# Performance work log

Hardware: AMD Instinct MI355X
Metric: run time of the kernel (lower is better)

The kernel has to match this reference:

```python
import jax, jax.numpy as jnp
import numpy as np

DIM = 64  # per-head dim used for the sqrt scale


def setup_inputs() -> dict:
    key = jax.random.key(0)
    kq, kk, kv, ke, kf = jax.random.split(key, 5)
    B, N, d, k = 32, 4096, 64, 256
    Q = jax.random.normal(kq, (B, N, d), dtype=jnp.float32)
    K = jax.random.normal(kk, (B, N, d), dtype=jnp.float32)
    V = jax.random.normal(kv, (B, N, d), dtype=jnp.float32)
    E = jax.random.normal(ke, (N, k), dtype=jnp.float32) * (1.0 / np.sqrt(N))
    F = jax.random.normal(kf, (N, k), dtype=jnp.float32) * (1.0 / np.sqrt(N))
    return {"Q": Q, "K": K, "V": V, "E": E, "F": F}


def reference(Q, K, V, E, F):
    # Linformer head: K^T E -> [B,d,k]; Q (K^T E) / sqrt(d) -> [B,N,k]
    K_proj = jnp.einsum('bnd,nk->bdk', K, E)          # low-rank key projection
    scores = jnp.einsum('bnd,bdk->bnk', Q, K_proj) / jnp.sqrt(jnp.float32(DIM))
    P_bar = jax.nn.softmax(scores, axis=2)            # [B,N,k]
    # (V^T F)^T -> [B,k,d]
    V_proj = jnp.einsum('bnd,nk->bkd', V, F)
    return jnp.einsum('bnk,bkd->bnd', P_bar, V_proj)  # [B,N,d]
```

## Files before the change

kernel.cpp:

```cpp
#include <hip/hip_runtime.h>
#include <hip/hip_bf16.h>

#define BB 32
#define NN 4096
#define DDIM 64
#define KKR 256

typedef __attribute__((ext_vector_type(8)))  short bf16x8;
typedef __attribute__((ext_vector_type(16))) float f32x16;
typedef __attribute__((ext_vector_type(4)))  float f32x4;

static __device__ inline unsigned short f2bf(float x) {
  union { float f; unsigned u; } v; v.f = x;
  unsigned r = (v.u + 0x7FFFu + ((v.u >> 16) & 1u)) >> 16;
  return (unsigned short)r;
}

__global__ __launch_bounds__(256) void pass0_kernel(
    const float* __restrict__ K, const float* __restrict__ V,
    const float* __restrict__ E, const float* __restrict__ F,
    unsigned short* __restrict__ KT, unsigned short* __restrict__ VT,
    unsigned short* __restrict__ ET, unsigned short* __restrict__ FT)
{
  const int id = blockIdx.x;
  const int t  = threadIdx.x;
  const float* src; unsigned short* dst; int stride, n0, col0;
  if (id < 2048) {
    int b = id >> 6, nt = id & 63;
    src = K + (long)b * NN * DDIM; dst = KT + (long)b * DDIM * NN;
    stride = 64; n0 = nt * 64; col0 = 0;
  } else if (id < 4096) {
    int i2 = id - 2048; int b = i2 >> 6, nt = i2 & 63;
    src = V + (long)b * NN * DDIM; dst = VT + (long)b * DDIM * NN;
    stride = 64; n0 = nt * 64; col0 = 0;
  } else if (id < 4352) {
    int i2 = id - 4096; int nt = i2 >> 2, ct = i2 & 3;
    src = E; dst = ET; stride = 256; n0 = nt * 64; col0 = ct * 64;
  } else {
    int i2 = id - 4352; int nt = i2 >> 2, ct = i2 & 3;
    src = F; dst = FT; stride = 256; n0 = nt * 64; col0 = ct * 64;
  }
  const int c = t & 63;
  const int q = t >> 6;
  const float* sp = src + (long)(n0 + q * 16) * stride + col0 + c;
  float v[16];
#pragma unroll
  for (int j = 0; j < 16; ++j) v[j] = sp[(long)j * stride];
  unsigned short o[16];
#pragma unroll
  for (int j = 0; j < 16; ++j) o[j] = f2bf(v[j]);
  unsigned short* dp = dst + (long)(col0 + c) * NN + n0 + q * 16;
#pragma unroll
  for (int j4 = 0; j4 < 4; ++j4)
    *(ushort4*)(dp + j4 * 4) = *(const ushort4*)&o[j4 * 4];
}

__global__ __launch_bounds__(256, 2) void proj_gemm(
    const unsigned short* __restrict__ KT, const unsigned short* __restrict__ VT,
    const unsigned short* __restrict__ ET, const unsigned short* __restrict__ FT,
    float* __restrict__ KpP, float* __restrict__ VpP)
{
  extern __shared__ unsigned short sm[];
  const int blk = blockIdx.x;
  const int chunk = blk & 3, mat = (blk >> 2) & 1, b = blk >> 3;
  const int t = threadIdx.x, w = t >> 6, l = t & 63, h = l >> 5, lr = l & 31;

  const unsigned short *Ag, *Bg; int M; float* Cg;
  if (mat == 0) {
    Ag = ET; Bg = KT + (long)b * DDIM * NN; M = 256;
    Cg = KpP + (long)chunk * (BB * 16384) + b * 16384;
  } else {
    Ag = VT + (long)b * DDIM * NN; Bg = FT; M = 64;
    Cg = VpP + (long)chunk * (BB * 16384) + b * 16384;
  }
  const int mt0 = (mat == 0) ? 2 * w : 0;
  const int nt0 = (mat == 0) ? 0 : 2 * w;

  f32x16 acc[2][2];
#pragma unroll
  for (int i = 0; i < 2; ++i)
#pragma unroll
    for (int j = 0; j < 2; ++j)
#pragma unroll
      for (int q = 0; q < 16; ++q) acc[i][j][q] = 0.f;

  const int n0 = chunk * 1024;
  for (int stg = 0; stg < 16; ++stg) {
    const int nb = n0 + stg * 64;
    __syncthreads();
#pragma unroll
    for (int i = 0; i < 10; ++i) {
      int cidx = i * 256 + t;
      int row = cidx >> 3, off = cidx & 7;
      const unsigned short* g =
          (row < M ? Ag + (long)row * NN : Bg + (long)(row - M) * NN) + nb + off * 8;
      *(bf16x8*)&sm[row * 72 + off * 8] = *(const bf16x8*)g;
    }
    __syncthreads();
#pragma unroll
    for (int kk = 0; kk < 4; ++kk) {
      bf16x8 a0 = *(const bf16x8*)&sm[(mt0 * 32 + lr) * 72 + kk * 16 + h * 8];
      bf16x8 a1 = *(const bf16x8*)&sm[((mt0 + 1) * 32 + lr) * 72 + kk * 16 + h * 8];
      bf16x8 b0 = *(const bf16x8*)&sm[(M + nt0 * 32 + lr) * 72 + kk * 16 + h * 8];
      bf16x8 b1 = *(const bf16x8*)&sm[(M + (nt0 + 1) * 32 + lr) * 72 + kk * 16 + h * 8];
      acc[0][0] = __builtin_amdgcn_mfma_f32_32x32x16_bf16(a0, b0, acc[0][0], 0, 0, 0);
      acc[0][1] = __builtin_amdgcn_mfma_f32_32x32x16_bf16(a0, b1, acc[0][1], 0, 0, 0);
      acc[1][0] = __builtin_amdgcn_mfma_f32_32x32x16_bf16(a1, b0, acc[1][0], 0, 0, 0);
      acc[1][1] = __builtin_amdgcn_mfma_f32_32x32x16_bf16(a1, b1, acc[1][1], 0, 0, 0);
    }
  }
#pragma unroll
  for (int mt = 0; mt < 2; ++mt)
#pragma unroll
    for (int nt = 0; nt < 2; ++nt)
#pragma unroll
      for (int i = 0; i < 16; ++i) {
        int row = (mt0 + mt) * 32 + (i & 3) + 8 * (i >> 2) + 4 * h;
        int col = (nt0 + nt) * 32 + lr;
        int idx = (mat == 0) ? row * 64 + col : row * 256 + col;
        Cg[idx] = acc[mt][nt][i];
      }
}

__global__ __launch_bounds__(256) void reduce_cvt(
    const float* __restrict__ KpP, const float* __restrict__ VpP,
    unsigned short* __restrict__ Kpb, unsigned short* __restrict__ Vpb)
{
  const int blk = blockIdx.x;
  const float* src = (blk < 256) ? KpP : VpP;
  unsigned short* dst = (blk < 256) ? Kpb : Vpb;
  const long i = (long)(blk & 255) * 2048 + threadIdx.x * 8;
  float a[8];
#pragma unroll
  for (int j = 0; j < 8; ++j) a[j] = 0.f;
#pragma unroll
  for (int cch = 0; cch < 4; ++cch) {
    const float4 p0 = *(const float4*)(src + (long)cch * (BB * 16384) + i);
    const float4 p1 = *(const float4*)(src + (long)cch * (BB * 16384) + i + 4);
    a[0] += p0.x; a[1] += p0.y; a[2] += p0.z; a[3] += p0.w;
    a[4] += p1.x; a[5] += p1.y; a[6] += p1.z; a[7] += p1.w;
  }
  unsigned short o[8];
#pragma unroll
  for (int j = 0; j < 8; ++j) o[j] = f2bf(a[j]);
  *(bf16x8*)(dst + i) = *(const bf16x8*)&o[0];
}

__global__ __launch_bounds__(256, 2) void attn2_kernel(
    const float* __restrict__ Qg, const unsigned short* __restrict__ Kpb,
    const unsigned short* __restrict__ Vpb, float* __restrict__ Og)
{
  extern __shared__ char smraw[];
  unsigned short* P = (unsigned short*)smraw;
  float* scr = (float*)(smraw + 65536);
  float* red = (float*)(smraw + 65536 + 8192);

  const int blk = blockIdx.x;
  const int b = blk >> 5, rg = blk & 31;
  const int t = threadIdx.x, w = t >> 6, l = t & 63, h = l >> 5, lr = l & 31;
  const int rh = w >> 1, ch = w & 1;

  const float* Qbase = Qg + ((long)b * NN + rg * 128) * 64;
  bf16x8 A[2][4];
#pragma unroll
  for (int rt = 0; rt < 2; ++rt)
#pragma unroll
    for (int kk = 0; kk < 4; ++kk) {
      const float* qp = Qbase + (long)(rh * 64 + rt * 32 + lr) * 64 + kk * 16 + h * 8;
      float4 x = *(const float4*)qp;
      float4 y = *(const float4*)(qp + 4);
      unsigned short u[8];
      u[0] = f2bf(x.x); u[1] = f2bf(x.y); u[2] = f2bf(x.z); u[3] = f2bf(x.w);
      u[4] = f2bf(y.x); u[5] = f2bf(y.y); u[6] = f2bf(y.z); u[7] = f2bf(y.w);
      A[rt][kk] = *(const bf16x8*)u;
    }

  const unsigned short* Kp = Kpb + (long)b * 16384;
  f32x16 acc[2][4];
#pragma unroll
  for (int rt = 0; rt < 2; ++rt)
#pragma unroll
    for (int ct = 0; ct < 4; ++ct)
#pragma unroll
      for (int q = 0; q < 16; ++q) acc[rt][ct][q] = 0.f;

  bf16x8 Bf[4], Bn[4];
#pragma unroll
  for (int ct = 0; ct < 4; ++ct)
    Bf[ct] = *(const bf16x8*)(Kp + (long)(ch * 128 + ct * 32 + lr) * 64 + h * 8);
#pragma unroll
  for (int kk = 0; kk < 4; ++kk) {
    if (kk < 3) {
#pragma unroll
      for (int ct = 0; ct < 4; ++ct)
        Bn[ct] = *(const bf16x8*)(Kp + (long)(ch * 128 + ct * 32 + lr) * 64 + (kk + 1) * 16 + h * 8);
    }
#pragma unroll
    for (int ct = 0; ct < 4; ++ct) {
      acc[0][ct] = __builtin_amdgcn_mfma_f32_32x32x16_bf16(A[0][kk], Bf[ct], acc[0][ct], 0, 0, 0);
      acc[1][ct] = __builtin_amdgcn_mfma_f32_32x32x16_bf16(A[1][kk], Bf[ct], acc[1][ct], 0, 0, 0);
    }
#pragma unroll
    for (int ct = 0; ct < 4; ++ct) Bf[ct] = Bn[ct];
  }

#pragma unroll
  for (int rt = 0; rt < 2; ++rt)
#pragma unroll
    for (int ct = 0; ct < 4; ++ct)
#pragma unroll
      for (int q = 0; q < 16; ++q)
        acc[rt][ct][q] = exp2f(acc[rt][ct][q] * 0.1803368801f);

  float ps[2][16];
#pragma unroll
  for (int rt = 0; rt < 2; ++rt)
#pragma unroll
    for (int q = 0; q < 16; ++q)
      ps[rt][q] = (acc[rt][0][q] + acc[rt][1][q]) + (acc[rt][2][q] + acc[rt][3][q]);
#pragma unroll
  for (int rt = 0; rt < 2; ++rt)
#pragma unroll
    for (int q = 0; q < 16; ++q) {
      ps[rt][q] += __shfl_xor(ps[rt][q], 8);
      ps[rt][q] += __shfl_xor(ps[rt][q], 16);
    }
  if (((l >> 3) & 3) == 0) {
#pragma unroll
    for (int rt = 0; rt < 2; ++rt)
#pragma unroll
      for (int q = 0; q < 16; ++q) {
        int rowL = (q & 3) + 8 * (q >> 2) + 4 * h;
        scr[w * 512 + (rt * 32 + rowL) * 8 + (l & 7)] = ps[rt][q];
      }
  }
  {
    const float* p = &scr[w * 512 + l * 8];
    f32x4 x = *(const f32x4*)p, y = *(const f32x4*)(p + 4);
    float s = (x[0] + x[1]) + (x[2] + x[3]) + (y[0] + y[1]) + (y[2] + y[3]);
    red[ch * 128 + rh * 64 + l] = s;
  }

#pragma unroll
  for (int rt = 0; rt < 2; ++rt)
#pragma unroll
    for (int ct = 0; ct < 4; ++ct)
#pragma unroll
      for (int q = 0; q < 16; ++q) {
        int rowL = rh * 64 + rt * 32 + (q & 3) + 8 * (q >> 2) + 4 * h;
        int col  = ch * 128 + ct * 32 + lr;
        int chk  = (col >> 3) ^ (rowL & 7);
        P[rowL * 256 + chk * 8 + (col & 7)] = f2bf(acc[rt][ct][q]);
      }
  __syncthreads();

  const unsigned short* Vp = Vpb + (long)b * 16384;
  f32x16 o[2];
#pragma unroll
  for (int rt = 0; rt < 2; ++rt)
#pragma unroll
    for (int q = 0; q < 16; ++q) o[rt][q] = 0.f;

#pragma unroll
  for (int kk = 0; kk < 16; ++kk) {
    bf16x8 Bv = *(const bf16x8*)(Vp + (long)(ch * 32 + lr) * 256 + kk * 16 + h * 8);
    bf16x8 Ap[2];
#pragma unroll
    for (int rt = 0; rt < 2; ++rt) {
      int rowL = rh * 64 + rt * 32 + lr;
      int col  = kk * 16 + h * 8;
      int chk  = (col >> 3) ^ (rowL & 7);
      Ap[rt] = *(const bf16x8*)&P[rowL * 256 + chk * 8];
    }
    o[0] = __builtin_amdgcn_mfma_f32_32x32x16_bf16(Ap[0], Bv, o[0], 0, 0, 0);
    o[1] = __builtin_amdgcn_mfma_f32_32x32x16_bf16(Ap[1], Bv, o[1], 0, 0, 0);
  }

#pragma unroll
  for (int rt = 0; rt < 2; ++rt)
#pragma unroll
    for (int ig = 0; ig < 4; ++ig) {
      int r0 = rh * 64 + rt * 32 + ig * 8 + 4 * h;
      f32x4 l0 = *(const f32x4*)&red[r0];
      f32x4 l1 = *(const f32x4*)&red[128 + r0];
#pragma unroll
      for (int j = 0; j < 4; ++j) {
        float val = o[rt][ig * 4 + j] * __builtin_amdgcn_rcpf(l0[j] + l1[j]);
        Og[((long)b * NN + rg * 128 + r0 + j) * 64 + ch * 32 + lr] = val;
      }
    }
}

extern "C" void kernel_launch(void* const* d_in, const int* in_sizes, int n_in,
                              void* d_out, int out_size, void* d_ws, size_t ws_size,
                              hipStream_t stream) {
  const float* Q = (const float*)d_in[0];
  const float* K = (const float*)d_in[1];
  const float* V = (const float*)d_in[2];
  const float* E = (const float*)d_in[3];
  const float* F = (const float*)d_in[4];
  float* out = (float*)d_out;

  char* ws = (char*)d_ws;
  float*          KpP = (float*)(ws);
  float*          VpP = (float*)(ws + (8l << 20));
  unsigned short* Kpb = (unsigned short*)(ws + (16l << 20));
  unsigned short* Vpb = (unsigned short*)(ws + (17l << 20));
  unsigned short* KT  = (unsigned short*)(ws + (18l << 20));
  unsigned short* VT  = (unsigned short*)(ws + (34l << 20));
  unsigned short* ET  = (unsigned short*)(ws + (50l << 20));
  unsigned short* FT  = (unsigned short*)(ws + (52l << 20));

  pass0_kernel<<<dim3(4608), dim3(256), 0, stream>>>(K, V, E, F, KT, VT, ET, FT);

  hipFuncSetAttribute((const void*)proj_gemm,
                      hipFuncAttributeMaxDynamicSharedMemorySize, 46080);
  proj_gemm<<<dim3(256), dim3(256), 46080, stream>>>(KT, VT, ET, FT, KpP, VpP);

  reduce_cvt<<<dim3(512), dim3(256), 0, stream>>>(KpP, VpP, Kpb, Vpb);

  hipFuncSetAttribute((const void*)attn2_kernel,
                      hipFuncAttributeMaxDynamicSharedMemorySize, 74752);
  attn2_kernel<<<dim3(1024), dim3(256), 74752, stream>>>(Q, Kpb, Vpb, out);
}
```

Before: 214.2 us.

## Keep attention probabilities in registers via transposed MFMA and coalesce output

Restructures the attention kernel so each wave owns 32 full rows, computing S^T = Kp·Q^T so that the exp'd probabilities can be repacked into bf16 MFMA operands with cross-half shuffles instead of a large LDS staging buffer. The row sum becomes a per-lane accumulation plus one shuffle, which removes the scratch reductions and the mid-kernel barrier. Output is staged through a swizzled LDS tile so global stores are float4-coalesced. The pass0 transpose store also uses 16-byte writes. The cost is a higher register footprint from holding 16 bf16x8 P fragments, and each wave now reloads all of Kp and Vp from global or cache.

```diff
diff --git a/kernel.cpp b/kernel.cpp
--- a/kernel.cpp
+++ b/kernel.cpp
@@ -14,6 +14,13 @@
   union { float f; unsigned u; } v; v.f = x;
   unsigned r = (v.u + 0x7FFFu + ((v.u >> 16) & 1u)) >> 16;
   return (unsigned short)r;
+}
+
+static __device__ inline unsigned packbf2(float a, float b) {
+  union { float f; unsigned u; } x, y; x.f = a; y.f = b;
+  unsigned ua = x.u + 0x7FFFu + ((x.u >> 16) & 1u);
+  unsigned ub = y.u + 0x7FFFu + ((y.u >> 16) & 1u);
+  return (ua >> 16) | (ub & 0xFFFF0000u);
 }
 
 __global__ __launch_bounds__(256) void pass0_kernel(
@@ -50,9 +57,8 @@
 #pragma unroll
   for (int j = 0; j < 16; ++j) o[j] = f2bf(v[j]);
   unsigned short* dp = dst + (long)(col0 + c) * NN + n0 + q * 16;
-#pragma unroll
-  for (int j4 = 0; j4 < 4; ++j4)
-    *(ushort4*)(dp + j4 * 4) = *(const ushort4*)&o[j4 * 4];
+  *(bf16x8*)dp       = *(const bf16x8*)&o[0];
+  *(bf16x8*)(dp + 8) = *(const bf16x8*)&o[8];
 }
 
 __global__ __launch_bounds__(256, 2) void proj_gemm(
@@ -150,145 +156,106 @@
     const float* __restrict__ Qg, const unsigned short* __restrict__ Kpb,
     const unsigned short* __restrict__ Vpb, float* __restrict__ Og)
 {
-  extern __shared__ char smraw[];
-  unsigned short* P = (unsigned short*)smraw;
-  float* scr = (float*)(smraw + 65536);
-  float* red = (float*)(smraw + 65536 + 8192);
+  __shared__ float O_lds[128 * 64];
 
   const int blk = blockIdx.x;
   const int b = blk >> 5, rg = blk & 31;
-  const int t = threadIdx.x, w = t >> 6, l = t & 63, h = l >> 5, lr = l & 31;
-  const int rh = w >> 1, ch = w & 1;
-
-  const float* Qbase = Qg + ((long)b * NN + rg * 128) * 64;
-  bf16x8 A[2][4];
-#pragma unroll
-  for (int rt = 0; rt < 2; ++rt)
+  const int t = threadIdx.x, w = t >> 6, l = t & 63;
+  const int h = l >> 5, lr = l & 31;
+  const int rbase = rg * 128 + w * 32;
+
+  const float* Qrow = Qg + ((long)b * NN + rbase + lr) * 64;
+  bf16x8 Bq[4];
+#pragma unroll
+  for (int kk = 0; kk < 4; ++kk) {
+    float4 x = *(const float4*)(Qrow + kk * 16 + h * 8);
+    float4 y = *(const float4*)(Qrow + kk * 16 + h * 8 + 4);
+    unsigned short u[8];
+    u[0] = f2bf(x.x); u[1] = f2bf(x.y); u[2] = f2bf(x.z); u[3] = f2bf(x.w);
+    u[4] = f2bf(y.x); u[5] = f2bf(y.y); u[6] = f2bf(y.z); u[7] = f2bf(y.w);
+    Bq[kk] = *(const bf16x8*)u;
+  }
+
+  const unsigned short* Kp = Kpb + (long)b * 16384;
+  const unsigned short* Vp = Vpb + (long)b * 16384;
+
+  union UV { uint4 u; bf16x8 v; };
+  bf16x8 Bp[16];
+  float rowpart = 0.f;
+
+#pragma unroll
+  for (int kt = 0; kt < 8; ++kt) {
+    f32x16 s;
+#pragma unroll
+    for (int q = 0; q < 16; ++q) s[q] = 0.f;
 #pragma unroll
     for (int kk = 0; kk < 4; ++kk) {
-      const float* qp = Qbase + (long)(rh * 64 + rt * 32 + lr) * 64 + kk * 16 + h * 8;
-      float4 x = *(const float4*)qp;
-      float4 y = *(const float4*)(qp + 4);
-      unsigned short u[8];
-      u[0] = f2bf(x.x); u[1] = f2bf(x.y); u[2] = f2bf(x.z); u[3] = f2bf(x.w);
-      u[4] = f2bf(y.x); u[5] = f2bf(y.y); u[6] = f2bf(y.z); u[7] = f2bf(y.w);
-      A[rt][kk] = *(const bf16x8*)u;
-    }
-
-  const unsigned short* Kp = Kpb + (long)b * 16384;
-  f32x16 acc[2][4];
-#pragma unroll
-  for (int rt = 0; rt < 2; ++rt)
-#pragma unroll
-    for (int ct = 0; ct < 4; ++ct)
-#pragma unroll
-      for (int q = 0; q < 16; ++q) acc[rt][ct][q] = 0.f;
-
-  bf16x8 Bf[4], Bn[4];
-#pragma unroll
-  for (int ct = 0; ct < 4; ++ct)
-    Bf[ct] = *(const bf16x8*)(Kp + (long)(ch * 128 + ct * 32 + lr) * 64 + h * 8);
-#pragma unroll
-  for (int kk = 0; kk < 4; ++kk) {
-    if (kk < 3) {
-#pragma unroll
-      for (int ct = 0; ct < 4; ++ct)
-        Bn[ct] = *(const bf16x8*)(Kp + (long)(ch * 128 + ct * 32 + lr) * 64 + (kk + 1) * 16 + h * 8);
-    }
-#pragma unroll
-    for (int ct = 0; ct < 4; ++ct) {
-      acc[0][ct] = __builtin_amdgcn_mfma_f32_32x32x16_bf16(A[0][kk], Bf[ct], acc[0][ct], 0, 0, 0);
-      acc[1][ct] = __builtin_amdgcn_mfma_f32_32x32x16_bf16(A[1][kk], Bf[ct], acc[1][ct], 0, 0, 0);
-    }
-#pragma unroll
-    for (int ct = 0; ct < 4; ++ct) Bf[ct] = Bn[ct];
-  }
-
-#pragma unroll
-  for (int rt = 0; rt < 2; ++rt)
-#pragma unroll
-    for (int ct = 0; ct < 4; ++ct)
-#pragma unroll
-      for (int q = 0; q < 16; ++q)
-        acc[rt][ct][q] = exp2f(acc[rt][ct][q] * 0.1803368801f);
-
-  float ps[2][16];
-#pragma unroll
-  for (int rt = 0; rt < 2; ++rt)
-#pragma unroll
-    for (int q = 0; q < 16; ++q)
-      ps[rt][q] = (acc[rt][0][q] + acc[rt][1][q]) + (acc[rt][2][q] + acc[rt][3][q]);
-#pragma unroll
-  for (int rt = 0; rt < 2; ++rt)
+      bf16x8 A = *(const bf16x8*)(Kp + (long)(kt * 32 + lr) * 64 + kk * 16 + h * 8);
+      s = __builtin_amdgcn_mfma_f32_32x32x16_bf16(A, Bq[kk], s, 0, 0, 0);
+    }
+    float p[16];
 #pragma unroll
     for (int q = 0; q < 16; ++q) {
-      ps[rt][q] += __shfl_xor(ps[rt][q], 8);
-      ps[rt][q] += __shfl_xor(ps[rt][q], 16);
-    }
-  if (((l >> 3) & 3) == 0) {
-#pragma unroll
-    for (int rt = 0; rt < 2; ++rt)
-#pragma unroll
-      for (int q = 0; q < 16; ++q) {
-        int rowL = (q & 3) + 8 * (q >> 2) + 4 * h;
-        scr[w * 512 + (rt * 32 + rowL) * 8 + (l & 7)] = ps[rt][q];
-      }
-  }
-  {
-    const float* p = &scr[w * 512 + l * 8];
-    f32x4 x = *(const f32x4*)p, y = *(const f32x4*)(p + 4);
-    float s = (x[0] + x[1]) + (x[2] + x[3]) + (y[0] + y[1]) + (y[2] + y[3]);
-    red[ch * 128 + rh * 64 + l] = s;
-  }
-
-#pragma unroll
-  for (int rt = 0; rt < 2; ++rt)
-#pragma unroll
-    for (int ct = 0; ct < 4; ++ct)
-#pragma unroll
-      for (int q = 0; q < 16; ++q) {
-        int rowL = rh * 64 + rt * 32 + (q & 3) + 8 * (q >> 2) + 4 * h;
-        int col  = ch * 128 + ct * 32 + lr;
-        int chk  = (col >> 3) ^ (rowL & 7);
-        P[rowL * 256 + chk * 8 + (col & 7)] = f2bf(acc[rt][ct][q]);
-      }
+      p[q] = exp2f(s[q] * 0.1803368801f);
+      rowpart += p[q];
+    }
+    unsigned wv[8];
+#pragma unroll
+    for (int m = 0; m < 8; ++m) wv[m] = packbf2(p[2 * m], p[2 * m + 1]);
+    unsigned r02 = __shfl_xor(h ? wv[0] : wv[2], 32);
+    unsigned r13 = __shfl_xor(h ? wv[1] : wv[3], 32);
+    unsigned r46 = __shfl_xor(h ? wv[4] : wv[6], 32);
+    unsigned r57 = __shfl_xor(h ? wv[5] : wv[7], 32);
+    UV c0, c1;
+    if (h == 0) {
+      c0.u = uint4{wv[0], wv[1], r02, r13};
+      c1.u = uint4{wv[4], wv[5], r46, r57};
+    } else {
+      c0.u = uint4{r02, r13, wv[2], wv[3]};
+      c1.u = uint4{r46, r57, wv[6], wv[7]};
+    }
+    Bp[kt * 2 + 0] = c0.v;
+    Bp[kt * 2 + 1] = c1.v;
+  }
+  float rowsum = rowpart + __shfl_xor(rowpart, 32);
+
+  f32x16 o[2];
+#pragma unroll
+  for (int mt = 0; mt < 2; ++mt)
+#pragma unroll
+    for (int q = 0; q < 16; ++q) o[mt][q] = 0.f;
+#pragma unroll
+  for (int kc = 0; kc < 16; ++kc) {
+    bf16x8 A0 = *(const bf16x8*)(Vp + (long)lr * 256 + kc * 16 + h * 8);
+    bf16x8 A1 = *(const bf16x8*)(Vp + (long)(32 + lr) * 256 + kc * 16 + h * 8);
+    o[0] = __builtin_amdgcn_mfma_f32_32x32x16_bf16(A0, Bp[kc], o[0], 0, 0, 0);
+    o[1] = __builtin_amdgcn_mfma_f32_32x32x16_bf16(A1, Bp[kc], o[1], 0, 0, 0);
+  }
+
+  const float inv = __builtin_amdgcn_rcpf(rowsum);
+  const int r = w * 32 + lr;
+#pragma unroll
+  for (int mt = 0; mt < 2; ++mt)
+#pragma unroll
+    for (int qg = 0; qg < 4; ++qg) {
+      f32x4 vq;
+      vq[0] = o[mt][qg * 4 + 0] * inv;
+      vq[1] = o[mt][qg * 4 + 1] * inv;
+      vq[2] = o[mt][qg * 4 + 2] * inv;
+      vq[3] = o[mt][qg * 4 + 3] * inv;
+      int cd = 8 * mt + 2 * qg + h;
+      int cp = cd ^ (r & 15);
+      *(f32x4*)&O_lds[r * 64 + cp * 4] = vq;
+    }
   __syncthreads();
 
-  const unsigned short* Vp = Vpb + (long)b * 16384;
-  f32x16 o[2];
-#pragma unroll
-  for (int rt = 0; rt < 2; ++rt)
-#pragma unroll
-    for (int q = 0; q < 16; ++q) o[rt][q] = 0.f;
-
-#pragma unroll
-  for (int kk = 0; kk < 16; ++kk) {
-    bf16x8 Bv = *(const bf16x8*)(Vp + (long)(ch * 32 + lr) * 256 + kk * 16 + h * 8);
-    bf16x8 Ap[2];
-#pragma unroll
-    for (int rt = 0; rt < 2; ++rt) {
-      int rowL = rh * 64 + rt * 32 + lr;
-      int col  = kk * 16 + h * 8;
-      int chk  = (col >> 3) ^ (rowL & 7);
-      Ap[rt] = *(const bf16x8*)&P[rowL * 256 + chk * 8];
-    }
-    o[0] = __builtin_amdgcn_mfma_f32_32x32x16_bf16(Ap[0], Bv, o[0], 0, 0, 0);
-    o[1] = __builtin_amdgcn_mfma_f32_32x32x16_bf16(Ap[1], Bv, o[1], 0, 0, 0);
-  }
-
-#pragma unroll
-  for (int rt = 0; rt < 2; ++rt)
-#pragma unroll
-    for (int ig = 0; ig < 4; ++ig) {
-      int r0 = rh * 64 + rt * 32 + ig * 8 + 4 * h;
-      f32x4 l0 = *(const f32x4*)&red[r0];
-      f32x4 l1 = *(const f32x4*)&red[128 + r0];
-#pragma unroll
-      for (int j = 0; j < 4; ++j) {
-        float val = o[rt][ig * 4 + j] * __builtin_amdgcn_rcpf(l0[j] + l1[j]);
-        Og[((long)b * NN + rg * 128 + r0 + j) * 64 + ch * 32 + lr] = val;
-      }
-    }
+  const long obase = ((long)b * NN + rg * 128) * 64;
+#pragma unroll
+  for (int i = 0; i < 8; ++i) {
+    int ci = i * 256 + t;
+    int rr = ci >> 4, cc = ci & 15, cp = cc ^ (rr & 15);
+    *(float4*)(Og + obase + rr * 64 + cc * 4) = *(const float4*)&O_lds[rr * 64 + cp * 4];
+  }
 }
 
 extern "C" void kernel_launch(void* const* d_in, const int* in_sizes, int n_in,
@@ -319,7 +286,5 @@
 
   reduce_cvt<<<dim3(512), dim3(256), 0, stream>>>(KpP, VpP, Kpb, Vpb);
 
-  hipFuncSetAttribute((const void*)attn2_kernel,
-                      hipFuncAttributeMaxDynamicSharedMemorySize, 74752);
-  attn2_kernel<<<dim3(1024), dim3(256), 74752, stream>>>(Q, Kpb, Vpb, out);
-}
+  attn2_kernel<<<dim3(1024), dim3(256), 0, stream>>>(Q, Kpb, Vpb, out);
+}
```

New measurement: 221.8 us. 1.04x slower.
